# Kernel optimization log

Measured on AMD Instinct MI355X. Metric: run time of the kernel, lower is better.

The kernel has to match this reference:

```python
import jax, jax.numpy as jnp
import numpy as np

HIDDEN = 4096
N_HEADS = 32
N_KV_HEADS = 8
HEAD_DIM = HIDDEN // N_HEADS  # 128
N_GROUPS = N_HEADS // N_KV_HEADS  # 4
ROPE_THETA = 10000.0
NEG_INF = -1e9


def fake_quant(x):
    """Symmetric per-tensor int8 fake quantization (quantize -> dequantize)."""
    scale = jnp.maximum(jnp.max(jnp.abs(x)) / 127.0, 1e-8)
    return jnp.clip(jnp.round(x / scale), -127.0, 127.0) * scale


def q_linear(x, W):
    # torch Linear: y = x @ W.T ; both operands fake-quantized (dequant-inline GEMM)
    return jnp.einsum('bsh,oh->bso', fake_quant(x), fake_quant(W))


def rope_cos_sin(position_ids, head_dim, dtype):
    inv_freq = 1.0 / (ROPE_THETA ** (jnp.arange(0, head_dim, 2, dtype=jnp.float32) / head_dim))
    freqs = position_ids.astype(jnp.float32)[..., None] * inv_freq  # [b, s, hd/2]
    emb = jnp.concatenate([freqs, freqs], axis=-1)                   # [b, s, hd]
    return jnp.cos(emb).astype(dtype), jnp.sin(emb).astype(dtype)


def rotate_half(x):
    x1, x2 = jnp.split(x, 2, axis=-1)
    return jnp.concatenate([-x2, x1], axis=-1)


def setup_inputs() -> dict:
    key = jax.random.key(0)
    ks = jax.random.split(key, 6)
    b, s = 2, 1024
    hidden_states = jax.random.normal(ks[0], (b, s, HIDDEN), dtype=jnp.float32)
    # additive causal mask [b, 1, q, kv]
    causal = jnp.where(jnp.tril(jnp.ones((s, s), dtype=bool)), 0.0, NEG_INF).astype(jnp.float32)
    attention_mask = jnp.broadcast_to(causal[None, None], (b, 1, s, s))
    position_ids = jnp.broadcast_to(jnp.arange(s, dtype=jnp.int64)[None, :], (b, s))
    winit = 1.0 / np.sqrt(HIDDEN)
    Wq = jax.random.normal(ks[1], (HIDDEN, HIDDEN), dtype=jnp.float32) * winit
    Wk = jax.random.normal(ks[2], (N_KV_HEADS * HEAD_DIM, HIDDEN), dtype=jnp.float32) * winit
    Wv = jax.random.normal(ks[3], (N_KV_HEADS * HEAD_DIM, HIDDEN), dtype=jnp.float32) * winit
    Wo = jax.random.normal(ks[4], (HIDDEN, HIDDEN), dtype=jnp.float32) * winit
    return {"hidden_states": hidden_states, "attention_mask": attention_mask,
            "position_ids": position_ids, "Wq": Wq, "Wk": Wk, "Wv": Wv, "Wo": Wo}


def reference(hidden_states, attention_mask, position_ids, Wq, Wk, Wv, Wo):
    b, s, _ = hidden_states.shape
    dtype = hidden_states.dtype

    # quantized QKV projections
    q = q_linear(hidden_states, Wq).reshape(b, s, N_HEADS, HEAD_DIM).transpose(0, 2, 1, 3)
    k = q_linear(hidden_states, Wk).reshape(b, s, N_KV_HEADS, HEAD_DIM).transpose(0, 2, 1, 3)
    v = q_linear(hidden_states, Wv).reshape(b, s, N_KV_HEADS, HEAD_DIM).transpose(0, 2, 1, 3)

    # RoPE
    cos, sin = rope_cos_sin(position_ids, HEAD_DIM, dtype)  # [b, s, hd]
    cos, sin = cos[:, None], sin[:, None]                   # broadcast over heads
    q = q * cos + rotate_half(q) * sin
    k = k * cos + rotate_half(k) * sin

    # GQA: repeat kv heads
    k = jnp.repeat(k, N_GROUPS, axis=1)  # [b, H, s, hd]
    v = jnp.repeat(v, N_GROUPS, axis=1)

    # quantized QK^T (per-tensor fake quant on both operands)
    attn = jnp.einsum('bhqd,bhkd->bhqk', fake_quant(q), fake_quant(k)) / jnp.sqrt(
        jnp.asarray(HEAD_DIM, dtype=jnp.float32)).astype(dtype)
    attn = attn + attention_mask
    attn = jax.nn.softmax(attn.astype(jnp.float32), axis=-1).astype(dtype)
    # attention_dropout = 0.0 (inference)

    # quantized AV matmul
    out = jnp.einsum('bhqk,bhkd->bhqd', fake_quant(attn), fake_quant(v))
    out = out.transpose(0, 2, 1, 3).reshape(b, s, HIDDEN)
    out = q_linear(out, Wo)
    return out
```

## Files before the change

kernel.cpp:

```cpp
#include <hip/hip_runtime.h>
#include <math.h>

#define B_ 2
#define S_ 1024
#define HID 4096
#define NH 32
#define NKV 8
#define HD 128
#define LOG2E 1.44269504088896340736f

typedef short s16x8 __attribute__((ext_vector_type(8)));
typedef float f32x4 __attribute__((ext_vector_type(4)));
typedef int i32x4 __attribute__((ext_vector_type(4)));
typedef unsigned short u16;
typedef u16 u16x4 __attribute__((ext_vector_type(4)));
typedef signed char s8;

__device__ __forceinline__ f32x4 mfma16(s16x8 a, s16x8 b, f32x4 c) {
  return __builtin_amdgcn_mfma_f32_16x16x32_bf16(a, b, c, 0, 0, 0);
}
__device__ __forceinline__ i32x4 mfma_i8(i32x4 a, i32x4 b, i32x4 c) {
  return __builtin_amdgcn_mfma_i32_16x16x64_i8(a, b, c, 0, 0, 0);
}
__device__ __forceinline__ u16 f2bf(float f) {
  union { float f; unsigned u; } v; v.f = f;
  return (u16)(v.u >> 16);
}
__device__ __forceinline__ float get_scale(const unsigned* sc, int slot) {
  return fmaxf(__uint_as_float(sc[slot]) / 127.0f, 1e-8f);
}
__device__ __forceinline__ int q127(float x, float s) {
  return (int)fminf(fmaxf(rintf(x / s), -127.f), 127.f);
}
__device__ __forceinline__ unsigned pack4(float4 v, float s) {
  return (q127(v.x, s) & 255) | ((q127(v.y, s) & 255) << 8) |
         ((q127(v.z, s) & 255) << 16) | ((q127(v.w, s) & 255) << 24);
}
__device__ __forceinline__ float max4(float4 v) {
  return fmaxf(fmaxf(fabsf(v.x), fabsf(v.y)), fmaxf(fabsf(v.z), fabsf(v.w)));
}
__device__ __forceinline__ void gload16(const void* g, void* l) {
  __builtin_amdgcn_global_load_lds(
      (const __attribute__((address_space(1))) unsigned*)g,
      (__attribute__((address_space(3))) unsigned*)l, 16, 0, 0);
}
__device__ __forceinline__ void atomic_absmax(unsigned* out, float m, int lane) {
  #pragma unroll
  for (int o = 32; o >= 1; o >>= 1) m = fmaxf(m, __shfl_xor(m, o));
  if (lane == 0) atomicMax(out, __float_as_uint(m));
}

#define SB_() __builtin_amdgcn_sched_barrier(0)
#define PBAR() do { SB_(); __builtin_amdgcn_s_barrier(); SB_(); } while (0)
#define VM6() do { SB_(); asm volatile("s_waitcnt vmcnt(6)" ::: "memory"); } while (0)
#define VM0() do { SB_(); asm volatile("s_waitcnt vmcnt(0)" ::: "memory"); } while (0)

__device__ __forceinline__ void tensor_pick(int blk, int& r, int& b0, int& nb) {
  if (blk < 342)       { r = 0; b0 = 0;    nb = 342; }
  else if (blk < 1024) { r = 1; b0 = 342;  nb = 682; }
  else if (blk < 1195) { r = 2; b0 = 1024; nb = 171; }
  else if (blk < 1366) { r = 3; b0 = 1195; nb = 171; }
  else                 { r = 4; b0 = 1366; nb = 682; }
}

__global__ void absmax5_k(const float4* __restrict__ p0, const float4* __restrict__ p1,
                          const float4* __restrict__ p2, const float4* __restrict__ p3,
                          const float4* __restrict__ p4, unsigned* __restrict__ sc) {
  int r, b0, nb;
  tensor_pick(blockIdx.x, r, b0, nb);
  const float4* x; int n4;
  if (r == 0)      { x = p0; n4 = B_ * S_ * HID / 4; }
  else if (r == 1) { x = p1; n4 = HID * HID / 4; }
  else if (r == 2) { x = p2; n4 = NKV * HD * HID / 4; }
  else if (r == 3) { x = p3; n4 = NKV * HD * HID / 4; }
  else             { x = p4; n4 = HID * HID / 4; }
  const int stride = nb * 256;
  int i = (blockIdx.x - b0) * 256 + threadIdx.x;
  float m0 = 0.f, m1 = 0.f, m2 = 0.f, m3 = 0.f;
  for (; i + 3 * stride < n4; i += 4 * stride) {
    float4 v0 = x[i], v1 = x[i + stride], v2 = x[i + 2 * stride], v3 = x[i + 3 * stride];
    m0 = fmaxf(m0, max4(v0)); m1 = fmaxf(m1, max4(v1));
    m2 = fmaxf(m2, max4(v2)); m3 = fmaxf(m3, max4(v3));
  }
  for (; i < n4; i += stride) m0 = fmaxf(m0, max4(x[i]));
  float m = fmaxf(fmaxf(m0, m1), fmaxf(m2, m3));
  atomic_absmax(sc + r, m, threadIdx.x & 63);
}

__global__ void quant5_k(const float4* __restrict__ p0, const float4* __restrict__ p1,
                         const float4* __restrict__ p2, const float4* __restrict__ p3,
                         const float4* __restrict__ p4,
                         unsigned* __restrict__ y0, unsigned* __restrict__ y1,
                         unsigned* __restrict__ y2, unsigned* __restrict__ y3,
                         unsigned* __restrict__ y4, const unsigned* __restrict__ sc) {
  int r, b0, nb;
  tensor_pick(blockIdx.x, r, b0, nb);
  const float4* x; unsigned* y; int n4;
  if (r == 0)      { x = p0; y = y0; n4 = B_ * S_ * HID / 4; }
  else if (r == 1) { x = p1; y = y1; n4 = HID * HID / 4; }
  else if (r == 2) { x = p2; y = y2; n4 = NKV * HD * HID / 4; }
  else if (r == 3) { x = p3; y = y3; n4 = NKV * HD * HID / 4; }
  else             { x = p4; y = y4; n4 = HID * HID / 4; }
  float s = get_scale(sc, r);
  const int stride = nb * 256;
  int i = (blockIdx.x - b0) * 256 + threadIdx.x;
  for (; i + 3 * stride < n4; i += 4 * stride) {
    float4 v0 = x[i], v1 = x[i + stride], v2 = x[i + 2 * stride], v3 = x[i + 3 * stride];
    y[i] = pack4(v0, s);
    y[i + stride] = pack4(v1, s);
    y[i + 2 * stride] = pack4(v2, s);
    y[i + 3 * stride] = pack4(v3, s);
  }
  for (; i < n4; i += stride) y[i] = pack4(x[i], s);
}

__global__ void quant_k(const float4* __restrict__ x, unsigned* __restrict__ y, int n4,
                        const unsigned* __restrict__ sc, int slot) {
  float s = get_scale(sc, slot);
  int stride = gridDim.x * blockDim.x;
  int i = blockIdx.x * blockDim.x + threadIdx.x;
  for (; i + 3 * stride < n4; i += 4 * stride) {
    float4 v0 = x[i], v1 = x[i + stride], v2 = x[i + 2 * stride], v3 = x[i + 3 * stride];
    y[i] = pack4(v0, s);
    y[i + stride] = pack4(v1, s);
    y[i + 2 * stride] = pack4(v2, s);
    y[i + 3 * stride] = pack4(v3, s);
  }
  for (; i < n4; i += stride) y[i] = pack4(x[i], s);
}

__global__ void add_k(const float4* __restrict__ p0, const float4* __restrict__ p1,
                      float4* __restrict__ out, int n4) {
  int stride = gridDim.x * blockDim.x;
  int i = blockIdx.x * blockDim.x + threadIdx.x;
  for (; i + stride < n4; i += 2 * stride) {
    float4 a0 = p0[i], b0 = p1[i], a1 = p0[i + stride], b1 = p1[i + stride];
    out[i] = make_float4(a0.x + b0.x, a0.y + b0.y, a0.z + b0.z, a0.w + b0.w);
    out[i + stride] = make_float4(a1.x + b1.x, a1.y + b1.y, a1.z + b1.z, a1.w + b1.w);
  }
  for (; i < n4; i += stride) {
    float4 a = p0[i], b = p1[i];
    out[i] = make_float4(a.x + b.x, a.y + b.y, a.z + b.z, a.w + b.w);
  }
}

__device__ __forceinline__ void rdA(const s8* slot, int wm, int lr, int lg,
                                    i32x4 af[4][2]) {
  #pragma unroll
  for (int mi = 0; mi < 4; ++mi) {
    int row = wm * 64 + mi * 16 + lr;
    const char* base = (const char*)slot + row * 128;
    int sw = (row & 7) << 4;
    #pragma unroll
    for (int ks = 0; ks < 2; ++ks)
      af[mi][ks] = *(const i32x4*)(base + ((ks * 64 + lg * 16) ^ sw));
  }
}
__device__ __forceinline__ void rdB(const s8* slot, int wn, int lr, int lg,
                                    i32x4 bf[2][2]) {
  #pragma unroll
  for (int ni = 0; ni < 2; ++ni) {
    int row = wn * 32 + ni * 16 + lr;
    const char* base = (const char*)slot + row * 128;
    int sw = (row & 7) << 4;
    #pragma unroll
    for (int ks = 0; ks < 2; ++ks)
      bf[ni][ks] = *(const i32x4*)(base + ((ks * 64 + lg * 16) ^ sw));
  }
}
template <int PM, int PN>
__device__ __forceinline__ void mfma_phase(i32x4 (&acc)[2][2][4][2],
                                           const i32x4 (&af)[4][2],
                                           const i32x4 (&bf)[2][2]) {
  __builtin_amdgcn_s_setprio(1);
  #pragma unroll
  for (int mi = 0; mi < 4; ++mi)
    #pragma unroll
    for (int ni = 0; ni < 2; ++ni)
      #pragma unroll
      for (int ks = 0; ks < 2; ++ks)
        acc[PM][PN][mi][ni] = mfma_i8(af[mi][ks], bf[ni][ks], acc[PM][PN][mi][ni]);
  __builtin_amdgcn_s_setprio(0);
}

__device__ void gemm256(const s8* __restrict__ A, const s8* __restrict__ Bm,
                        float* __restrict__ C, int Ncols, int m0, int n0,
                        int k0, int nkt, float scale, unsigned* omax, s8* S) {
  const int tid = threadIdx.x;
  const int wave = tid >> 6, lane = tid & 63;
  const int lr = lane & 15, lg = lane >> 4;
  const int wm = wave >> 2, wn = wave & 3;
  s8* SA00 = S;          s8* SA01 = S + 16384;
  s8* SB00 = S + 32768;  s8* SB01 = S + 49152;
  s8* SA10 = S + 65536;  s8* SA11 = S + 81920;
  s8* SB10 = S + 98304;  s8* SB11 = S + 114688;
  const int r0 = tid >> 3;
  const int ce = ((tid & 7) * 16) ^ ((r0 & 7) << 4);
  const s8* pa0 = A + (size_t)(m0 + r0) * HID + k0 + ce;
  const s8* pa1 = pa0 + (size_t)128 * HID;
  const s8* pb0 = Bm + (size_t)(n0 + r0) * HID + k0 + ce;
  const s8* pb1 = pb0 + (size_t)128 * HID;
  const int wdst = wave * 1024;
  i32x4 acc[2][2][4][2] = {};
  i32x4 af[4][2], bf[2][2];

  auto STG = [&](const s8* p, s8* slot, int tcol) {
    const s8* g = p + tcol * 128;
    gload16(g, slot + wdst);
    gload16(g + (size_t)64 * HID, slot + 8192 + wdst);
  };

  STG(pa0, SA00, 0); STG(pb0, SB00, 0); STG(pa1, SA01, 0); STG(pb1, SB01, 0);
  STG(pa0, SA10, 1); STG(pb1, SB11, 1); STG(pa1, SA11, 1);
  VM6(); PBAR();

  #pragma unroll 1
  for (int t = 0; t < nkt; t += 2) {
    const bool g2 = t + 2 < nkt, g3 = t + 3 < nkt;
    rdA(SA00, wm, lr, lg, af); rdB(SB00, wn, lr, lg, bf);
    STG(pb0, SB10, t + 1);
    PBAR(); mfma_phase<0, 0>(acc, af, bf); PBAR();
    rdB(SB01, wn, lr, lg, bf);
    if (g2) STG(pa0, SA00, t + 2);
    PBAR(); mfma_phase<0, 1>(acc, af, bf); PBAR();
    rdA(SA01, wm, lr, lg, af);
    if (g2) STG(pb1, SB01, t + 2);
    PBAR(); mfma_phase<1, 1>(acc, af, bf); PBAR();
    rdB(SB00, wn, lr, lg, bf);
    if (g2) STG(pa1, SA01, t + 2);
    PBAR(); mfma_phase<1, 0>(acc, af, bf);
    if (g2) { VM6(); } else { VM0(); }
    PBAR();
    rdA(SA10, wm, lr, lg, af); rdB(SB10, wn, lr, lg, bf);
    if (g2) STG(pb0, SB00, t + 2);
    PBAR(); mfma_phase<0, 0>(acc, af, bf); PBAR();
    rdB(SB11, wn, lr, lg, bf);
    if (g3) STG(pa0, SA10, t + 3);
    PBAR(); mfma_phase<0, 1>(acc, af, bf); PBAR();
    rdA(SA11, wm, lr, lg, af);
    if (g3) STG(pb1, SB11, t + 3);
    PBAR(); mfma_phase<1, 1>(acc, af, bf); PBAR();
    rdB(SB10, wn, lr, lg, bf);
    if (g3) STG(pa1, SA11, t + 3);
    PBAR(); mfma_phase<1, 0>(acc, af, bf); VM6(); PBAR();
  }

  float gm = 0.f;
  #pragma unroll
  for (int mh = 0; mh < 2; ++mh)
    #pragma unroll
    for (int nh = 0; nh < 2; ++nh)
      #pragma unroll
      for (int mi = 0; mi < 4; ++mi)
        #pragma unroll
        for (int ni = 0; ni < 2; ++ni) {
          size_t rbase = (size_t)(m0 + mh * 128 + wm * 64 + mi * 16 + lg * 4);
          int cb = n0 + nh * 128 + wn * 32 + ni * 16 + lr;
          #pragma unroll
          for (int r = 0; r < 4; ++r) {
            float v = (float)acc[mh][nh][mi][ni][r] * scale;
            gm = fmaxf(gm, fabsf(v));
            C[(rbase + r) * (size_t)Ncols + cb] = v;
          }
        }
  if (omax) atomic_absmax(omax, gm, lane);
}

__global__ __launch_bounds__(512, 1) void gemm_qkv8(
    const s8* __restrict__ Xq, const s8* __restrict__ Wqb,
    const s8* __restrict__ Wkb, const s8* __restrict__ Wvb,
    float* __restrict__ qf, float* __restrict__ kf, float* __restrict__ vf,
    const unsigned* __restrict__ sc, unsigned* __restrict__ vmax) {
  extern __shared__ __align__(16) s8 S[];
  int raw = blockIdx.x;
  int wg = (raw & 7) * 24 + (raw >> 3);
  int bx = wg & 7, by = wg >> 3;
  const s8* Bm; float* C; int Ncols, n0, sslot; unsigned* om = nullptr;
  if (by < 16)      { Bm = Wqb; C = qf; Ncols = HID;      n0 = by * 256;        sslot = 1; }
  else if (by < 20) { Bm = Wkb; C = kf; Ncols = NKV * HD; n0 = (by - 16) * 256; sslot = 2; }
  else              { Bm = Wvb; C = vf; Ncols = NKV * HD; n0 = (by - 20) * 256; sslot = 3; om = vmax; }
  float scale = get_scale(sc, 0) * get_scale(sc, sslot);
  gemm256(Xq, Bm, C, Ncols, bx * 256, n0, 0, 32, scale, om, S);
}

__global__ __launch_bounds__(512, 1) void gemm_o8(
    const s8* __restrict__ A, const s8* __restrict__ Bm,
    float* __restrict__ P0, float* __restrict__ P1,
    const unsigned* __restrict__ sc) {
  extern __shared__ __align__(16) s8 S[];
  int raw = blockIdx.x;
  int wg = (raw & 7) * 32 + (raw >> 3);
  int tile = wg >> 1, half = wg & 1;
  int by = tile & 15, bx = tile >> 4;
  float scale = get_scale(sc, 8) * get_scale(sc, 4);
  gemm256(A, Bm, half ? P1 : P0, HID, bx * 256, by * 256, half * 2048, 16,
          scale, nullptr, S);
}

__global__ void rope_tab_k(float2* __restrict__ tab) {
  int i = blockIdx.x * 256 + threadIdx.x;
  int pos = i >> 6, d = i & 63;
  float inv = exp2f((float)d * (-13.287712379549449f / 64.0f));
  float ang = (float)pos * inv;
  tab[i] = make_float2(cosf(ang), sinf(ang));
}

__global__ void rope2_k(float* __restrict__ qf, float* __restrict__ kf,
                        unsigned* __restrict__ sc, const float2* __restrict__ tab) {
  int reg = blockIdx.y;
  float* q = reg ? kf : qf;
  int nheads = reg ? NKV : NH;
  unsigned* om = sc + (reg ? 6 : 5);
  int total = B_ * S_ * nheads * 16;
  int stride = gridDim.x * blockDim.x;
  float m = 0.f;
  for (int i = blockIdx.x * blockDim.x + threadIdx.x; i < total; i += stride) {
    int g = i & 15;
    int h = (i >> 4) % nheads;
    int bs = i / (16 * nheads);
    int pos = bs & (S_ - 1);
    size_t base = ((size_t)bs * nheads + h) * HD + g * 4;
    float4 x1 = *(float4*)(q + base);
    float4 x2 = *(float4*)(q + base + 64);
    const float4* t = (const float4*)(tab + ((size_t)pos << 6) + g * 4);
    float4 t0 = t[0], t1 = t[1];
    float4 o1, o2;
    o1.x = x1.x * t0.x - x2.x * t0.y;  o2.x = x2.x * t0.x + x1.x * t0.y;
    o1.y = x1.y * t0.z - x2.y * t0.w;  o2.y = x2.y * t0.z + x1.y * t0.w;
    o1.z = x1.z * t1.x - x2.z * t1.y;  o2.z = x2.z * t1.x + x1.z * t1.y;
    o1.w = x1.w * t1.z - x2.w * t1.w;  o2.w = x2.w * t1.z + x1.w * t1.w;
    *(float4*)(q + base) = o1;
    *(float4*)(q + base + 64) = o2;
    m = fmaxf(m, fmaxf(max4(o1), max4(o2)));
  }
  atomic_absmax(om, m, threadIdx.x & 63);
}

__global__ void quantqk_k(const float4* __restrict__ qf, const float4* __restrict__ kf,
                          unsigned* __restrict__ qq, unsigned* __restrict__ kq,
                          const unsigned* __restrict__ sc) {
  int reg = blockIdx.y;
  const float4* x = reg ? kf : qf;
  unsigned* y = reg ? kq : qq;
  int n4 = reg ? (B_ * S_ * NKV * HD / 4) : (B_ * S_ * HID / 4);
  float s = get_scale(sc, reg ? 6 : 5);
  int stride = gridDim.x * blockDim.x;
  int i = blockIdx.x * blockDim.x + threadIdx.x;
  for (; i + stride < n4; i += 2 * stride) {
    float4 v0 = x[i], v1 = x[i + stride];
    y[i] = pack4(v0, s);
    y[i + stride] = pack4(v1, s);
  }
  for (; i < n4; i += stride) y[i] = pack4(x[i], s);
}

__global__ __launch_bounds__(256) void vquant_t_k(const float* __restrict__ vf,
                                                  unsigned* __restrict__ vtw,
                                                  const unsigned* __restrict__ sc) {
  __shared__ u16 Ls[64 * 132];
  float s = get_scale(sc, 7);
  int st = blockIdx.x & 15, kvh = (blockIdx.x >> 4) & 7, b = blockIdx.x >> 7;
  int s0 = st * 64;
  #pragma unroll
  for (int i = 0; i < 8; ++i) {
    int o = i * 256 + threadIdx.x;
    int sr = o >> 5, c4 = o & 31;
    float4 v = *(const float4*)(vf + ((size_t)(b * S_ + s0 + sr)) * (NKV * HD) +
                                kvh * HD + c4 * 4);
    u16x4 w;
    w[0] = f2bf(fminf(fmaxf(rintf(v.x / s), -127.f), 127.f));
    w[1] = f2bf(fminf(fmaxf(rintf(v.y / s), -127.f), 127.f));
    w[2] = f2bf(fminf(fmaxf(rintf(v.z / s), -127.f), 127.f));
    w[3] = f2bf(fminf(fmaxf(rintf(v.w / s), -127.f), 127.f));
    *(u16x4*)(Ls + sr * 132 + c4 * 4) = w;
  }
  __syncthreads();
  #pragma unroll
  for (int i = 0; i < 16; ++i) {
    int o = i * 256 + threadIdx.x;
    int d = o >> 5, sj = o & 31;
    unsigned lo = Ls[(sj * 2) * 132 + d], hi = Ls[(sj * 2 + 1) * 132 + d];
    vtw[(((size_t)(b * NKV + kvh) * HD + d) << 9) + st * 32 + sj] = lo | (hi << 16);
  }
}

__global__ __launch_bounds__(512) void attn_k(
    const s8* __restrict__ Q, const s8* __restrict__ Kq, const u16* __restrict__ Vt,
    float* __restrict__ O, const unsigned* __restrict__ sc, unsigned* __restrict__ omax) {
  __shared__ __align__(16) s8 Ks[2][64 * 128];
  __shared__ __align__(16) u16 Vs[2][128 * 64];
  __shared__ __align__(16) u16 Ps[128 * 64];
  const int tid = threadIdx.x;
  const int wave = tid >> 6, lane = tid & 63;
  const int lr = lane & 15, lg = lane >> 4;
  const int raw = blockIdx.x;
  const int xcd = raw & 7, j = raw >> 3;
  const int grp = xcd + 8 * (j >> 4);
  const int within = j & 15;
  const int b = grp >> 3, kvh = grp & 7;
  const int h = kvh * 4 + (within >> 2);
  const int qp = within & 3;
  const float sq = get_scale(sc, 5), sk = get_scale(sc, 6), sv = get_scale(sc, 7);
  const float c2 = sq * sk * 0.08838834764831845f * LOG2E;
  const float M0 = 32.0f;
  const int k_row = tid >> 3;
  const int k_cb = ((tid & 7) * 16) ^ ((k_row & 7) << 4);
  const int v_rin = lane >> 3;
  const int v_cb = ((lane & 7) * 16) ^ ((v_rin & 7) << 4);
  float gmax = 0.f;

  auto stageK = [&](int buf, int kt) {
    gload16(Kq + (size_t)(b * S_ + kt * 64 + k_row) * (NKV * HD) + kvh * HD + k_cb,
            Ks[buf] + wave * 1024);
  };
  auto stageV = [&](int buf, int kt) {
    #pragma unroll
    for (int i = 0; i < 2; ++i) {
      int ch = wave * 2 + i;
      int vrow = ch * 8 + v_rin;
      gload16(Vt + ((size_t)(b * NKV + kvh) * HD + vrow) * S_ + kt * 64 + (v_cb >> 1),
              Vs[buf] + ch * 512);
    }
  };

  for (int pi = 0; pi < 2; ++pi) {
    const int qt = pi ? 7 - qp : qp;
    const int q0 = qt * 128;
    const int nkt = 2 * (qt + 1);
    const int qwmin = q0 + wave * 16;
    i32x4 aq[2];
    {
      const s8* qp_ = Q + (size_t)(b * S_ + q0 + wave * 16 + lr) * HID + h * HD + lg * 16;
      aq[0] = *(const i32x4*)(qp_);
      aq[1] = *(const i32x4*)(qp_ + 64);
    }
    float ll[4] = {0.f, 0.f, 0.f, 0.f};

    stageK(0, 0);
    __syncthreads();
    for (int kt = 0; kt < nkt; ++kt) {
      const int p = kt & 1;
      if (kt < nkt - 1) stageK(p ^ 1, kt + 1);
      i32x4 sacc[4] = {};
      __builtin_amdgcn_s_setprio(1);
      #pragma unroll
      for (int ks = 0; ks < 2; ++ks)
        #pragma unroll
        for (int n = 0; n < 4; ++n) {
          int row = n * 16 + lr;
          i32x4 bk = *(const i32x4*)((const char*)Ks[p] + row * 128 +
                                     ((ks * 64 + lg * 16) ^ ((row & 7) << 4)));
          sacc[n] = mfma_i8(aq[ks], bk, sacc[n]);
        }
      __builtin_amdgcn_s_setprio(0);
      if (kt * 64 + 63 <= qwmin) {
        #pragma unroll
        for (int r = 0; r < 4; ++r)
          #pragma unroll
          for (int n = 0; n < 4; ++n)
            ll[r] += exp2f(fmaf((float)sacc[n][r], c2, -M0));
      } else {
        #pragma unroll
        for (int r = 0; r < 4; ++r) {
          int qg = qwmin + lg * 4 + r;
          #pragma unroll
          for (int n = 0; n < 4; ++n) {
            int kg = kt * 64 + n * 16 + lr;
            float e = exp2f(fmaf((float)sacc[n][r], c2, -M0));
            ll[r] += (kg <= qg) ? e : 0.f;
          }
        }
      }
      __syncthreads();
    }
    float bias[4];
    #pragma unroll
    for (int r = 0; r < 4; ++r) {
      float l = ll[r];
      #pragma unroll
      for (int o = 8; o >= 1; o >>= 1) l += __shfl_xor(l, o);
      bias[r] = 6.9886846867721655f - __log2f(l) - M0;
    }

    f32x4 oacc[8] = {};
    stageK(0, 0); stageV(0, 0);
    __syncthreads();
    for (int kt = 0; kt < nkt; ++kt) {
      const int p = kt & 1;
      if (kt < nkt - 1) { stageK(p ^ 1, kt + 1); stageV(p ^ 1, kt + 1); }
      i32x4 sacc[4] = {};
      __builtin_amdgcn_s_setprio(1);
      #pragma unroll
      for (int ks = 0; ks < 2; ++ks)
        #pragma unroll
        for (int n = 0; n < 4; ++n) {
          int row = n * 16 + lr;
          i32x4 bk = *(const i32x4*)((const char*)Ks[p] + row * 128 +
                                     ((ks * 64 + lg * 16) ^ ((row & 7) << 4)));
          sacc[n] = mfma_i8(aq[ks], bk, sacc[n]);
        }
      __builtin_amdgcn_s_setprio(0);
      if (kt * 64 + 63 <= qwmin) {
        #pragma unroll
        for (int r = 0; r < 4; ++r) {
          int prow = wave * 16 + lg * 4 + r;
          #pragma unroll
          for (int n = 0; n < 4; ++n) {
            float p127 = rintf(exp2f(fmaf((float)sacc[n][r], c2, bias[r])));
            int col = n * 16 + lr;
            *(u16*)((char*)Ps + prow * 128 + ((col * 2) ^ ((prow & 7) << 4))) = f2bf(p127);
          }
        }
      } else {
        #pragma unroll
        for (int r = 0; r < 4; ++r) {
          int prow = wave * 16 + lg * 4 + r;
          int qg = qwmin + lg * 4 + r;
          #pragma unroll
          for (int n = 0; n < 4; ++n) {
            int kg = kt * 64 + n * 16 + lr;
            float a = fmaf((float)sacc[n][r], c2, bias[r]);
            float p127 = (kg <= qg) ? rintf(exp2f(a)) : 0.f;
            int col = n * 16 + lr;
            *(u16*)((char*)Ps + prow * 128 + ((col * 2) ^ ((prow & 7) << 4))) = f2bf(p127);
          }
        }
      }
      __builtin_amdgcn_s_setprio(1);
      #pragma unroll
      for (int ks = 0; ks < 2; ++ks) {
        int prow = wave * 16 + lr;
        s16x8 ap = *(const s16x8*)((const char*)Ps + prow * 128 +
                                   ((ks * 64 + lg * 16) ^ ((prow & 7) << 4)));
        #pragma unroll
        for (int n = 0; n < 8; ++n) {
          int vrow = n * 16 + lr;
          s16x8 bv = *(const s16x8*)((const char*)Vs[p] + vrow * 128 +
                                     ((ks * 64 + lg * 16) ^ ((vrow & 7) << 4)));
          oacc[n] = mfma16(ap, bv, oacc[n]);
        }
      }
      __builtin_amdgcn_s_setprio(0);
      __syncthreads();
    }
    const float pvs = sv * (1.0f / 127.0f);
    #pragma unroll
    for (int n = 0; n < 8; ++n)
      #pragma unroll
      for (int r = 0; r < 4; ++r) {
        float v = oacc[n][r] * pvs;
        gmax = fmaxf(gmax, fabsf(v));
        O[(size_t)(b * S_ + q0 + wave * 16 + lg * 4 + r) * HID + h * HD + n * 16 + lr] = v;
      }
  }
  atomic_absmax(omax, gmax, lane);
}

extern "C" void kernel_launch(void* const* d_in, const int* in_sizes, int n_in,
                              void* d_out, int out_size, void* d_ws, size_t ws_size,
                              hipStream_t stream) {
  const float* hs = (const float*)d_in[0];
  const float* Wq = (const float*)d_in[3];
  const float* Wk = (const float*)d_in[4];
  const float* Wv = (const float*)d_in[5];
  const float* Wo = (const float*)d_in[6];
  float* out = (float*)d_out;
  char* ws = (char*)d_ws;

  unsigned* sc = (unsigned*)ws;
  size_t off = 256;
  s8* Xq = (s8*)(ws + off); off += (size_t)B_ * S_ * HID;
  size_t wqb_off = off;
  s8* Wqb = (s8*)(ws + off); off += (size_t)HID * HID;
  s8* Wkb = (s8*)(ws + off); off += (size_t)NKV * HD * HID;
  s8* Wvb = (s8*)(ws + off); off += (size_t)NKV * HD * HID;
  s8* Wob = (s8*)(ws + off); off += (size_t)HID * HID;
  size_t qf_off = off;
  float* qf = (float*)(ws + off); off += (size_t)B_ * S_ * HID * 4;
  float* kf = (float*)(ws + off); off += (size_t)B_ * S_ * NKV * HD * 4;
  float* vf = (float*)(ws + off); off += (size_t)B_ * S_ * NKV * HD * 4;
  s8* qq = (s8*)(ws + off); off += (size_t)B_ * S_ * HID;
  s8* kq = (s8*)(ws + off); off += (size_t)B_ * S_ * NKV * HD;
  u16* vt = (u16*)(ws + off); off += (size_t)B_ * S_ * NKV * HD * 2;
  float2* tab = (float2*)(ws + off); off += (size_t)S_ * 64 * 8;
  float* P1 = (float*)(ws + off); off += (size_t)B_ * S_ * HID * 4;
  float* attnf = (float*)(ws + qf_off);
  s8* attnq = (s8*)(ws + wqb_off);
  float* P0 = (float*)(ws + qf_off);

  hipFuncSetAttribute((const void*)gemm_qkv8,
                      hipFuncAttributeMaxDynamicSharedMemorySize, 131072);
  hipFuncSetAttribute((const void*)gemm_o8,
                      hipFuncAttributeMaxDynamicSharedMemorySize, 131072);

  hipMemsetAsync(sc, 0, 64, stream);

  dim3 blk(256);
  absmax5_k<<<2048, blk, 0, stream>>>(
      (const float4*)hs, (const float4*)Wq, (const float4*)Wk,
      (const float4*)Wv, (const float4*)Wo, sc);
  quant5_k<<<2048, blk, 0, stream>>>(
      (const float4*)hs, (const float4*)Wq, (const float4*)Wk,
      (const float4*)Wv, (const float4*)Wo,
      (unsigned*)Xq, (unsigned*)Wqb, (unsigned*)Wkb, (unsigned*)Wvb,
      (unsigned*)Wob, sc);
  rope_tab_k<<<256, blk, 0, stream>>>(tab);

  gemm_qkv8<<<192, 512, 131072, stream>>>(Xq, Wqb, Wkb, Wvb, qf, kf, vf, sc, sc + 7);

  rope2_k<<<dim3(512, 2), blk, 0, stream>>>(qf, kf, sc, tab);
  quantqk_k<<<dim3(512, 2), blk, 0, stream>>>((const float4*)qf, (const float4*)kf,
                                              (unsigned*)qq, (unsigned*)kq, sc);
  vquant_t_k<<<256, blk, 0, stream>>>(vf, (unsigned*)vt, sc);

  attn_k<<<256, 512, 0, stream>>>(qq, kq, vt, attnf, sc, sc + 8);

  quant_k<<<2048, blk, 0, stream>>>((const float4*)attnf, (unsigned*)attnq,
                                    B_ * S_ * HID / 4, sc, 8);
  gemm_o8<<<256, 512, 131072, stream>>>(attnq, Wob, P0, P1, sc);
  add_k<<<2048, blk, 0, stream>>>((const float4*)P0, (const float4*)P1,
                                  (float4*)out, B_ * S_ * HID / 4);
}
```

Before: 449.9 us.

## Switch attention PV matmul from bf16 to int8 MFMA with repacked V layout

The P·V product in the attention kernel now runs on int8 16x16x64 MFMA instead of bf16 16x16x32, with P stored as int8 in shared memory and V quantized, transposed and pre-swizzled into an int8 layout matching the new fragment reads. This halves V and P storage and bandwidth and halves the number of PV MFMA issues per tile. The elementwise quant/add kernels are also rewritten so each thread handles four contiguous float4s and writes one 16-byte vector, instead of strided scalar stores. Int8 accumulation is exact for these values, but the new swizzle and layout must stay consistent between vquant_t_k and attn_k.

```diff
diff --git a/kernel.cpp b/kernel.cpp
--- a/kernel.cpp
+++ b/kernel.cpp
@@ -13,18 +13,11 @@
 typedef float f32x4 __attribute__((ext_vector_type(4)));
 typedef int i32x4 __attribute__((ext_vector_type(4)));
 typedef unsigned short u16;
-typedef u16 u16x4 __attribute__((ext_vector_type(4)));
+typedef unsigned uint4v __attribute__((ext_vector_type(4)));
 typedef signed char s8;
 
-__device__ __forceinline__ f32x4 mfma16(s16x8 a, s16x8 b, f32x4 c) {
-  return __builtin_amdgcn_mfma_f32_16x16x32_bf16(a, b, c, 0, 0, 0);
-}
 __device__ __forceinline__ i32x4 mfma_i8(i32x4 a, i32x4 b, i32x4 c) {
   return __builtin_amdgcn_mfma_i32_16x16x64_i8(a, b, c, 0, 0, 0);
-}
-__device__ __forceinline__ u16 f2bf(float f) {
-  union { float f; unsigned u; } v; v.f = f;
-  return (u16)(v.u >> 16);
 }
 __device__ __forceinline__ float get_scale(const unsigned* sc, int slot) {
   return fmaxf(__uint_as_float(sc[slot]) / 127.0f, 1e-8f);
@@ -74,15 +67,15 @@
   else if (r == 2) { x = p2; n4 = NKV * HD * HID / 4; }
   else if (r == 3) { x = p3; n4 = NKV * HD * HID / 4; }
   else             { x = p4; n4 = HID * HID / 4; }
+  const int ng = n4 >> 2;
   const int stride = nb * 256;
-  int i = (blockIdx.x - b0) * 256 + threadIdx.x;
   float m0 = 0.f, m1 = 0.f, m2 = 0.f, m3 = 0.f;
-  for (; i + 3 * stride < n4; i += 4 * stride) {
-    float4 v0 = x[i], v1 = x[i + stride], v2 = x[i + 2 * stride], v3 = x[i + 3 * stride];
+  for (int g = (blockIdx.x - b0) * 256 + threadIdx.x; g < ng; g += stride) {
+    const float4* p = x + g * 4;
+    float4 v0 = p[0], v1 = p[1], v2 = p[2], v3 = p[3];
     m0 = fmaxf(m0, max4(v0)); m1 = fmaxf(m1, max4(v1));
     m2 = fmaxf(m2, max4(v2)); m3 = fmaxf(m3, max4(v3));
   }
-  for (; i < n4; i += stride) m0 = fmaxf(m0, max4(x[i]));
   float m = fmaxf(fmaxf(m0, m1), fmaxf(m2, m3));
   atomic_absmax(sc + r, m, threadIdx.x & 63);
 }
@@ -102,45 +95,47 @@
   else if (r == 3) { x = p3; y = y3; n4 = NKV * HD * HID / 4; }
   else             { x = p4; y = y4; n4 = HID * HID / 4; }
   float s = get_scale(sc, r);
+  const int ng = n4 >> 2;
   const int stride = nb * 256;
-  int i = (blockIdx.x - b0) * 256 + threadIdx.x;
-  for (; i + 3 * stride < n4; i += 4 * stride) {
-    float4 v0 = x[i], v1 = x[i + stride], v2 = x[i + 2 * stride], v3 = x[i + 3 * stride];
-    y[i] = pack4(v0, s);
-    y[i + stride] = pack4(v1, s);
-    y[i + 2 * stride] = pack4(v2, s);
-    y[i + 3 * stride] = pack4(v3, s);
-  }
-  for (; i < n4; i += stride) y[i] = pack4(x[i], s);
+  for (int g = (blockIdx.x - b0) * 256 + threadIdx.x; g < ng; g += stride) {
+    const float4* p = x + g * 4;
+    float4 v0 = p[0], v1 = p[1], v2 = p[2], v3 = p[3];
+    uint4v o;
+    o[0] = pack4(v0, s); o[1] = pack4(v1, s);
+    o[2] = pack4(v2, s); o[3] = pack4(v3, s);
+    *(uint4v*)(y + g * 4) = o;
+  }
 }
 
 __global__ void quant_k(const float4* __restrict__ x, unsigned* __restrict__ y, int n4,
                         const unsigned* __restrict__ sc, int slot) {
   float s = get_scale(sc, slot);
+  const int ng = n4 >> 2;
   int stride = gridDim.x * blockDim.x;
-  int i = blockIdx.x * blockDim.x + threadIdx.x;
-  for (; i + 3 * stride < n4; i += 4 * stride) {
-    float4 v0 = x[i], v1 = x[i + stride], v2 = x[i + 2 * stride], v3 = x[i + 3 * stride];
-    y[i] = pack4(v0, s);
-    y[i + stride] = pack4(v1, s);
-    y[i + 2 * stride] = pack4(v2, s);
-    y[i + 3 * stride] = pack4(v3, s);
-  }
-  for (; i < n4; i += stride) y[i] = pack4(x[i], s);
+  for (int g = blockIdx.x * blockDim.x + threadIdx.x; g < ng; g += stride) {
+    const float4* p = x + g * 4;
+    float4 v0 = p[0], v1 = p[1], v2 = p[2], v3 = p[3];
+    uint4v o;
+    o[0] = pack4(v0, s); o[1] = pack4(v1, s);
+    o[2] = pack4(v2, s); o[3] = pack4(v3, s);
+    *(uint4v*)(y + g * 4) = o;
+  }
 }
 
 __global__ void add_k(const float4* __restrict__ p0, const float4* __restrict__ p1,
                       float4* __restrict__ out, int n4) {
+  const int ng = n4 >> 2;
   int stride = gridDim.x * blockDim.x;
-  int i = blockIdx.x * blockDim.x + threadIdx.x;
-  for (; i + stride < n4; i += 2 * stride) {
-    float4 a0 = p0[i], b0 = p1[i], a1 = p0[i + stride], b1 = p1[i + stride];
-    out[i] = make_float4(a0.x + b0.x, a0.y + b0.y, a0.z + b0.z, a0.w + b0.w);
-    out[i + stride] = make_float4(a1.x + b1.x, a1.y + b1.y, a1.z + b1.z, a1.w + b1.w);
-  }
-  for (; i < n4; i += stride) {
-    float4 a = p0[i], b = p1[i];
-    out[i] = make_float4(a.x + b.x, a.y + b.y, a.z + b.z, a.w + b.w);
+  for (int g = blockIdx.x * blockDim.x + threadIdx.x; g < ng; g += stride) {
+    const float4* a = p0 + g * 4;
+    const float4* b = p1 + g * 4;
+    float4 a0 = a[0], a1 = a[1], a2 = a[2], a3 = a[3];
+    float4 b0 = b[0], b1 = b[1], b2 = b[2], b3 = b[3];
+    float4* o = out + g * 4;
+    o[0] = make_float4(a0.x + b0.x, a0.y + b0.y, a0.z + b0.z, a0.w + b0.w);
+    o[1] = make_float4(a1.x + b1.x, a1.y + b1.y, a1.z + b1.z, a1.w + b1.w);
+    o[2] = make_float4(a2.x + b2.x, a2.y + b2.y, a2.z + b2.z, a2.w + b2.w);
+    o[3] = make_float4(a3.x + b3.x, a3.y + b3.y, a3.z + b3.z, a3.w + b3.w);
   }
 }
 
@@ -344,20 +339,22 @@
   unsigned* y = reg ? kq : qq;
   int n4 = reg ? (B_ * S_ * NKV * HD / 4) : (B_ * S_ * HID / 4);
   float s = get_scale(sc, reg ? 6 : 5);
+  const int ng = n4 >> 2;
   int stride = gridDim.x * blockDim.x;
-  int i = blockIdx.x * blockDim.x + threadIdx.x;
-  for (; i + stride < n4; i += 2 * stride) {
-    float4 v0 = x[i], v1 = x[i + stride];
-    y[i] = pack4(v0, s);
-    y[i + stride] = pack4(v1, s);
-  }
-  for (; i < n4; i += stride) y[i] = pack4(x[i], s);
+  for (int g = blockIdx.x * blockDim.x + threadIdx.x; g < ng; g += stride) {
+    const float4* p = x + g * 4;
+    float4 v0 = p[0], v1 = p[1], v2 = p[2], v3 = p[3];
+    uint4v o;
+    o[0] = pack4(v0, s); o[1] = pack4(v1, s);
+    o[2] = pack4(v2, s); o[3] = pack4(v3, s);
+    *(uint4v*)(y + g * 4) = o;
+  }
 }
 
 __global__ __launch_bounds__(256) void vquant_t_k(const float* __restrict__ vf,
-                                                  unsigned* __restrict__ vtw,
+                                                  s8* __restrict__ vt,
                                                   const unsigned* __restrict__ sc) {
-  __shared__ u16 Ls[64 * 132];
+  __shared__ __align__(16) s8 Ls[64][132];
   float s = get_scale(sc, 7);
   int st = blockIdx.x & 15, kvh = (blockIdx.x >> 4) & 7, b = blockIdx.x >> 7;
   int s0 = st * 64;
@@ -367,29 +364,31 @@
     int sr = o >> 5, c4 = o & 31;
     float4 v = *(const float4*)(vf + ((size_t)(b * S_ + s0 + sr)) * (NKV * HD) +
                                 kvh * HD + c4 * 4);
-    u16x4 w;
-    w[0] = f2bf(fminf(fmaxf(rintf(v.x / s), -127.f), 127.f));
-    w[1] = f2bf(fminf(fmaxf(rintf(v.y / s), -127.f), 127.f));
-    w[2] = f2bf(fminf(fmaxf(rintf(v.z / s), -127.f), 127.f));
-    w[3] = f2bf(fminf(fmaxf(rintf(v.w / s), -127.f), 127.f));
-    *(u16x4*)(Ls + sr * 132 + c4 * 4) = w;
+    *(unsigned*)(&Ls[sr][c4 * 4]) =
+        (q127(v.x, s) & 255) | ((q127(v.y, s) & 255) << 8) |
+        ((q127(v.z, s) & 255) << 16) | ((q127(v.w, s) & 255) << 24);
   }
   __syncthreads();
+  s8* base = vt + (size_t)(b * NKV + kvh) * 131072 + st * 128;
   #pragma unroll
-  for (int i = 0; i < 16; ++i) {
+  for (int i = 0; i < 8; ++i) {
     int o = i * 256 + threadIdx.x;
-    int d = o >> 5, sj = o & 31;
-    unsigned lo = Ls[(sj * 2) * 132 + d], hi = Ls[(sj * 2 + 1) * 132 + d];
-    vtw[(((size_t)(b * NKV + kvh) * HD + d) << 9) + st * 32 + sj] = lo | (hi << 16);
+    int j = o >> 5, half = (o >> 4) & 1, w = o & 15;
+    int d = 2 * j + half;
+    unsigned pk = (unsigned)(unsigned char)Ls[4 * w + 0][d] |
+                  ((unsigned)(unsigned char)Ls[4 * w + 1][d] << 8) |
+                  ((unsigned)(unsigned char)Ls[4 * w + 2][d] << 16) |
+                  ((unsigned)(unsigned char)Ls[4 * w + 3][d] << 24);
+    *(unsigned*)(base + (size_t)j * 2048 + half * 64 + ((w * 4) ^ ((j & 3) << 4))) = pk;
   }
 }
 
 __global__ __launch_bounds__(512) void attn_k(
-    const s8* __restrict__ Q, const s8* __restrict__ Kq, const u16* __restrict__ Vt,
+    const s8* __restrict__ Q, const s8* __restrict__ Kq, const s8* __restrict__ Vt,
     float* __restrict__ O, const unsigned* __restrict__ sc, unsigned* __restrict__ omax) {
   __shared__ __align__(16) s8 Ks[2][64 * 128];
-  __shared__ __align__(16) u16 Vs[2][128 * 64];
-  __shared__ __align__(16) u16 Ps[128 * 64];
+  __shared__ __align__(16) s8 Vs[2][64 * 128];
+  __shared__ __align__(16) s8 Ps[128 * 64];
   const int tid = threadIdx.x;
   const int wave = tid >> 6, lane = tid & 63;
   const int lr = lane & 15, lg = lane >> 4;
@@ -405,8 +404,8 @@
   const float M0 = 32.0f;
   const int k_row = tid >> 3;
   const int k_cb = ((tid & 7) * 16) ^ ((k_row & 7) << 4);
-  const int v_rin = lane >> 3;
-  const int v_cb = ((lane & 7) * 16) ^ ((v_rin & 7) << 4);
+  const s8* vbase = Vt + (size_t)(b * NKV + kvh) * 131072 +
+                    (size_t)(tid >> 3) * 2048 + (tid & 7) * 16;
   float gmax = 0.f;
 
   auto stageK = [&](int buf, int kt) {
@@ -414,13 +413,7 @@
             Ks[buf] + wave * 1024);
   };
   auto stageV = [&](int buf, int kt) {
-    #pragma unroll
-    for (int i = 0; i < 2; ++i) {
-      int ch = wave * 2 + i;
-      int vrow = ch * 8 + v_rin;
-      gload16(Vt + ((size_t)(b * NKV + kvh) * HD + vrow) * S_ + kt * 64 + (v_cb >> 1),
-              Vs[buf] + ch * 512);
-    }
+    gload16(vbase + kt * 128, Vs[buf] + wave * 1024);
   };
 
   for (int pi = 0; pi < 2; ++pi) {
@@ -482,7 +475,7 @@
       bias[r] = 6.9886846867721655f - __log2f(l) - M0;
     }
 
-    f32x4 oacc[8] = {};
+    i32x4 oacc[8] = {};
     stageK(0, 0); stageV(0, 0);
     __syncthreads();
     for (int kt = 0; kt < nkt; ++kt) {
@@ -504,11 +497,11 @@
         #pragma unroll
         for (int r = 0; r < 4; ++r) {
           int prow = wave * 16 + lg * 4 + r;
+          s8* pr = Ps + prow * 64;
           #pragma unroll
           for (int n = 0; n < 4; ++n) {
             float p127 = rintf(exp2f(fmaf((float)sacc[n][r], c2, bias[r])));
-            int col = n * 16 + lr;
-            *(u16*)((char*)Ps + prow * 128 + ((col * 2) ^ ((prow & 7) << 4))) = f2bf(p127);
+            pr[((n * 16) ^ (lg << 4)) + lr] = (s8)(int)p127;
           }
         }
       } else {
@@ -516,28 +509,26 @@
         for (int r = 0; r < 4; ++r) {
           int prow = wave * 16 + lg * 4 + r;
           int qg = qwmin + lg * 4 + r;
+          s8* pr = Ps + prow * 64;
           #pragma unroll
           for (int n = 0; n < 4; ++n) {
             int kg = kt * 64 + n * 16 + lr;
             float a = fmaf((float)sacc[n][r], c2, bias[r]);
             float p127 = (kg <= qg) ? rintf(exp2f(a)) : 0.f;
-            int col = n * 16 + lr;
-            *(u16*)((char*)Ps + prow * 128 + ((col * 2) ^ ((prow & 7) << 4))) = f2bf(p127);
+            pr[((n * 16) ^ (lg << 4)) + lr] = (s8)(int)p127;
           }
         }
       }
       __builtin_amdgcn_s_setprio(1);
-      #pragma unroll
-      for (int ks = 0; ks < 2; ++ks) {
-        int prow = wave * 16 + lr;
-        s16x8 ap = *(const s16x8*)((const char*)Ps + prow * 128 +
-                                   ((ks * 64 + lg * 16) ^ ((prow & 7) << 4)));
+      {
+        i32x4 ap = *(const i32x4*)(Ps + (wave * 16 + lr) * 64 +
+                                   ((lg * 16) ^ (((lr >> 2) & 3) << 4)));
         #pragma unroll
         for (int n = 0; n < 8; ++n) {
-          int vrow = n * 16 + lr;
-          s16x8 bv = *(const s16x8*)((const char*)Vs[p] + vrow * 128 +
-                                     ((ks * 64 + lg * 16) ^ ((vrow & 7) << 4)));
-          oacc[n] = mfma16(ap, bv, oacc[n]);
+          int jd = n * 8 + (lr >> 1);
+          i32x4 bv = *(const i32x4*)((const char*)Vs[p] + jd * 128 + (lr & 1) * 64 +
+                                     ((lg * 16) ^ ((jd & 3) << 4)));
+          oacc[n] = mfma_i8(ap, bv, oacc[n]);
         }
       }
       __builtin_amdgcn_s_setprio(0);
@@ -548,7 +539,7 @@
     for (int n = 0; n < 8; ++n)
       #pragma unroll
       for (int r = 0; r < 4; ++r) {
-        float v = oacc[n][r] * pvs;
+        float v = (float)oacc[n][r] * pvs;
         gmax = fmaxf(gmax, fabsf(v));
         O[(size_t)(b * S_ + q0 + wave * 16 + lg * 4 + r) * HID + h * HD + n * 16 + lr] = v;
       }
@@ -581,7 +572,7 @@
   float* vf = (float*)(ws + off); off += (size_t)B_ * S_ * NKV * HD * 4;
   s8* qq = (s8*)(ws + off); off += (size_t)B_ * S_ * HID;
   s8* kq = (s8*)(ws + off); off += (size_t)B_ * S_ * NKV * HD;
-  u16* vt = (u16*)(ws + off); off += (size_t)B_ * S_ * NKV * HD * 2;
+  s8* vt = (s8*)(ws + off); off += (size_t)B_ * S_ * NKV * HD;
   float2* tab = (float2*)(ws + off); off += (size_t)S_ * 64 * 8;
   float* P1 = (float*)(ws + off); off += (size_t)B_ * S_ * HID * 4;
   float* attnf = (float*)(ws + qf_off);
@@ -611,7 +602,7 @@
   rope2_k<<<dim3(512, 2), blk, 0, stream>>>(qf, kf, sc, tab);
   quantqk_k<<<dim3(512, 2), blk, 0, stream>>>((const float4*)qf, (const float4*)kf,
                                               (unsigned*)qq, (unsigned*)kq, sc);
-  vquant_t_k<<<256, blk, 0, stream>>>(vf, (unsigned*)vt, sc);
+  vquant_t_k<<<256, blk, 0, stream>>>(vf, vt, sc);
 
   attn_k<<<256, 512, 0, stream>>>(qq, kq, vt, attnf, sc, sc + 8);
 
```

New measurement: 446.7 us. Within noise of the previous version (-0.7%).
